# Performance work log

Measured on AMD Instinct MI355X. Metric: run time of the kernel, lower is better.

The kernel has to match this reference:

```python
import jax, jax.numpy as jnp
import numpy as np

B, N, D, C = 64, 512, 1024, 4  # batch, num_electrodes, d_model, num_classes
H = D // 2


def setup_inputs() -> dict:
    key = jax.random.key(0)
    ks = jax.random.split(key, 16)
    s = 0.02
    return {
        "Q": jax.random.normal(ks[0], (B, N, D), jnp.float32),
        "K": jax.random.normal(ks[1], (B, N, D), jnp.float32),
        "V": jax.random.normal(ks[2], (B, N, D), jnp.float32),
        "electrode_ids": jnp.arange(N, dtype=jnp.int64 if jax.config.jax_enable_x64 else jnp.int32),
        "emb": jax.random.normal(ks[3], (N, D), jnp.float32) * s,
        "dw1": jax.random.normal(ks[4], (H, D), jnp.float32) * s,
        "db1": jnp.zeros((H,), jnp.float32),
        "dw2": jax.random.normal(ks[5], (1, H), jnp.float32) * s,
        "db2": jnp.zeros((1,), jnp.float32),
        "sw1": jax.random.normal(ks[6], (H, D), jnp.float32) * s,
        "sb1": jnp.zeros((H,), jnp.float32),
        "sw2": jax.random.normal(ks[7], (1, H), jnp.float32) * s,
        "sb2": jnp.zeros((1,), jnp.float32),
        "dopamine_scale": jnp.asarray(1.0, jnp.float32),
        "serotonin_scale": jnp.asarray(1.0, jnp.float32),
        "fc_w": jax.random.normal(ks[8], (C, N * D), jnp.float32) * s,
        "fc_b": jnp.zeros((C,), jnp.float32),
    }


def reference(Q, K, V, electrode_ids, emb, dw1, db1, dw2, db2,
              sw1, sb1, sw2, sb2, dopamine_scale, serotonin_scale, fc_w, fc_b):
    e = emb[electrode_ids]                       # [N, D]
    Q = Q + e
    K = K + e
    V = V + e
    scale = jnp.sqrt(jnp.asarray(D, jnp.float32))
    scores = jnp.einsum('bnd,bmd->bnm', Q, K) / scale          # [B, N, N]
    probs = jax.nn.softmax(scores, axis=-1)
    entropy = -jnp.sum(probs * jnp.log(probs + 1e-6), axis=-1)  # [B, N]

    # dopamine MLP on Q tokens (eval mode -> dropout is identity)
    dh = jax.nn.relu(jnp.einsum('bnd,hd->bnh', Q, dw1) + db1)
    dopamine = jax.nn.sigmoid(jnp.einsum('bnh,oh->bno', dh, dw2) + db2)[..., 0]  # [B, N]

    # serotonin MLP on entropy broadcast to D identical features:
    # Linear(entropy * ones(D)) == entropy * W1.sum(axis=1) + b1 (same math, no [B,N,D] temp)
    sh = jax.nn.relu(entropy[..., None] * jnp.sum(sw1, axis=1) + sb1)            # [B, N, H]
    serotonin = jax.nn.sigmoid(jnp.einsum('bnh,oh->bno', sh, sw2) + sb2)[..., 0]  # [B, N]

    mod = dopamine_scale * dopamine[..., None] - serotonin_scale * serotonin[..., None]
    ms = scores + mod
    mu = jnp.mean(ms, axis=-1, keepdims=True)
    sd = jnp.std(ms, axis=-1, keepdims=True, ddof=1)  # torch.std default is unbiased
    ms = (ms - mu) / (sd + 1e-6)
    probs2 = jax.nn.softmax(ms, axis=-1)
    attn_out = jnp.einsum('bnm,bmd->bnd', probs2, V)   # [B, N, D]
    flat = attn_out.reshape(attn_out.shape[0], -1)      # [B, N*D]
    return flat @ fc_w.T + fc_b                          # [B, C]
```

## Files before the change

### kernel.cpp

```cpp
#include <hip/hip_runtime.h>

#define NN 512
#define ND 1024
#define NDW 524288
#define NBATCH 64

typedef __attribute__((ext_vector_type(8))) __bf16 bf16x8;
typedef __attribute__((ext_vector_type(4))) float f32x4;
typedef unsigned short u16;
typedef unsigned int u32;

__device__ __forceinline__ u16 f2bf(float x) {
    u32 u = __float_as_uint(x);
    u = (u + 0x7fffu + ((u >> 16) & 1u)) >> 16;
    return (u16)u;
}
__device__ __forceinline__ float bf2f(u16 x) {
    return __uint_as_float(((u32)x) << 16);
}

union BF8 { bf16x8 v; u16 s[8]; };

__device__ __forceinline__ void dma16(const u16* g, const u16* l) {
    __builtin_amdgcn_global_load_lds(
        (const __attribute__((address_space(1))) u32*)(uintptr_t)g,
        (__attribute__((address_space(3))) u32*)(u32)(uintptr_t)l,
        16, 0, 0);
}

__global__ __launch_bounds__(256)
void nma_init_out(float* __restrict__ out, const float* __restrict__ fcb) {
    int t = threadIdx.x;
    if (t < NBATCH * 4) out[t] = fcb[t & 3];
}

__global__ __launch_bounds__(256)
void prep_ke(const float* __restrict__ K, const int* __restrict__ eid,
             const float* __restrict__ emb, u16* __restrict__ Ke) {
    size_t f = ((size_t)blockIdx.x * 256 + threadIdx.x) * 8;
    int n = (int)((f >> 10) & (NN - 1));
    int col = (int)(f & (ND - 1));
    const float* kp = K + f;
    const float* ep = emb + (size_t)eid[n] * ND + col;
    float4 k0 = *(const float4*)kp, k1 = *(const float4*)(kp + 4);
    float4 e0 = *(const float4*)ep, e1 = *(const float4*)(ep + 4);
    union { uint4 q; u16 s[8]; } o;
    o.s[0]=f2bf(k0.x+e0.x); o.s[1]=f2bf(k0.y+e0.y); o.s[2]=f2bf(k0.z+e0.z); o.s[3]=f2bf(k0.w+e0.w);
    o.s[4]=f2bf(k1.x+e1.x); o.s[5]=f2bf(k1.y+e1.y); o.s[6]=f2bf(k1.z+e1.z); o.s[7]=f2bf(k1.w+e1.w);
    *(uint4*)(Ke + f) = o.q;
}

__global__ __launch_bounds__(256)
void prep_vt(const float* __restrict__ V, const int* __restrict__ eid,
             const float* __restrict__ emb, u16* __restrict__ VT) {
    __shared__ u16 T[64 * 72];
    const int tid = threadIdx.x;
    const int b = blockIdx.z, d0 = blockIdx.y * 64, n0 = blockIdx.x * 64;
    {
        const int r = tid >> 2, cs = (tid & 3) * 16;
        const int n = n0 + r;
        const float* vp = V + ((size_t)b * NN + n) * ND + d0 + cs;
        const float* ep = emb + (size_t)eid[n] * ND + d0 + cs;
        #pragma unroll
        for (int j = 0; j < 4; ++j) {
            float4 v = *(const float4*)(vp + j * 4);
            float4 e = *(const float4*)(ep + j * 4);
            T[(cs + j*4 + 0) * 72 + r] = f2bf(v.x + e.x);
            T[(cs + j*4 + 1) * 72 + r] = f2bf(v.y + e.y);
            T[(cs + j*4 + 2) * 72 + r] = f2bf(v.z + e.z);
            T[(cs + j*4 + 3) * 72 + r] = f2bf(v.w + e.w);
        }
    }
    __syncthreads();
    {
        const int dr = tid >> 2, ms = (tid & 3) * 16;
        u16* dst = VT + ((size_t)b * ND + d0 + dr) * NN + n0 + ms;
        *(uint4*)dst       = *(const uint4*)&T[dr * 72 + ms];
        *(uint4*)(dst + 8) = *(const uint4*)&T[dr * 72 + ms + 8];
    }
}

__global__ __launch_bounds__(256, 2)
void nma_attn(const float* __restrict__ Q, const int* __restrict__ eid,
              const float* __restrict__ emb, const u16* __restrict__ Ke,
              const u16* __restrict__ VT, u16* __restrict__ O)
{
    __shared__ __align__(16) u16 KV[NN * 32];
    __shared__ __align__(16) u16 Ps[32 * 520];
    __shared__ float red[4][32][4];
    __shared__ float rowM[32], rowInv[32], rowRden[32];

    const int tid  = threadIdx.x;
    const int w    = tid >> 6;
    const int lane = tid & 63;
    const int q    = lane >> 4;
    const int l15  = lane & 15;
    const int bid  = blockIdx.x;
    const int jj   = bid >> 3;
    const int b    = (bid & 7) + ((jj >> 4) << 3);
    const int i0   = (jj & 15) * 32;
    const size_t bOff = (size_t)b * NN * ND;

    const float* Qrow0 = Q + bOff + (size_t)(i0 + l15) * ND;
    const float* Qrow1 = Q + bOff + (size_t)(i0 + 16 + l15) * ND;
    const float* Erow0 = emb + (size_t)eid[i0 + l15] * ND;
    const float* Erow1 = emb + (size_t)eid[i0 + 16 + l15] * ND;

    const u16* KeB = Ke + bOff;
    const u16* VTB = VT + (size_t)b * ND * NN;
    const int liw = w * 64 + lane;

    f32x4 acc[2][8];
    #pragma unroll
    for (int it = 0; it < 2; ++it)
        #pragma unroll
        for (int mt = 0; mt < 8; ++mt)
            acc[it][mt] = (f32x4){0.f, 0.f, 0.f, 0.f};

    for (int kc = 0; kc < 32; ++kc) {
        __syncthreads();
        #pragma unroll
        for (int ii = 0; ii < 8; ++ii) {
            const int li = ii * 256 + liw;
            const int m = li >> 2, seg = li & 3;
            dma16(KeB + (size_t)m * ND + kc * 32 + seg * 8,
                  &KV[(size_t)(ii * 256 + w * 64) * 8]);
        }
        BF8 a0u, a1u;
        {
            const int k0 = kc * 32 + q * 8;
            float4 x0 = *(const float4*)(Qrow0 + k0);
            float4 x1 = *(const float4*)(Qrow0 + k0 + 4);
            float4 e0 = *(const float4*)(Erow0 + k0);
            float4 e1 = *(const float4*)(Erow0 + k0 + 4);
            a0u.s[0] = f2bf(x0.x + e0.x); a0u.s[1] = f2bf(x0.y + e0.y);
            a0u.s[2] = f2bf(x0.z + e0.z); a0u.s[3] = f2bf(x0.w + e0.w);
            a0u.s[4] = f2bf(x1.x + e1.x); a0u.s[5] = f2bf(x1.y + e1.y);
            a0u.s[6] = f2bf(x1.z + e1.z); a0u.s[7] = f2bf(x1.w + e1.w);
            x0 = *(const float4*)(Qrow1 + k0);
            x1 = *(const float4*)(Qrow1 + k0 + 4);
            e0 = *(const float4*)(Erow1 + k0);
            e1 = *(const float4*)(Erow1 + k0 + 4);
            a1u.s[0] = f2bf(x0.x + e0.x); a1u.s[1] = f2bf(x0.y + e0.y);
            a1u.s[2] = f2bf(x0.z + e0.z); a1u.s[3] = f2bf(x0.w + e0.w);
            a1u.s[4] = f2bf(x1.x + e1.x); a1u.s[5] = f2bf(x1.y + e1.y);
            a1u.s[6] = f2bf(x1.z + e1.z); a1u.s[7] = f2bf(x1.w + e1.w);
        }
        __syncthreads();
        #pragma unroll
        for (int mt = 0; mt < 8; ++mt) {
            bf16x8 bf = *(const bf16x8*)&KV[(w * 128 + mt * 16 + l15) * 32 + q * 8];
            acc[0][mt] = __builtin_amdgcn_mfma_f32_16x16x32_bf16(a0u.v, bf, acc[0][mt], 0, 0, 0);
            acc[1][mt] = __builtin_amdgcn_mfma_f32_16x16x32_bf16(a1u.v, bf, acc[1][mt], 0, 0, 0);
        }
    }

    const float SC = 0.03125f;
    #pragma unroll
    for (int it = 0; it < 2; ++it)
        #pragma unroll
        for (int mt = 0; mt < 8; ++mt) {
            acc[it][mt][0] *= SC; acc[it][mt][1] *= SC;
            acc[it][mt][2] *= SC; acc[it][mt][3] *= SC;
        }
    float ssum[2][4], ssq[2][4], smax[2][4];
    #pragma unroll
    for (int it = 0; it < 2; ++it)
        #pragma unroll
        for (int r = 0; r < 4; ++r) {
            float s = 0.f, s2 = 0.f, mx = -3.4e38f;
            #pragma unroll
            for (int mt = 0; mt < 8; ++mt) {
                float v = acc[it][mt][r];
                s += v; s2 += v * v; mx = fmaxf(mx, v);
            }
            #pragma unroll
            for (int d = 1; d < 16; d <<= 1) {
                s  += __shfl_xor(s, d);
                s2 += __shfl_xor(s2, d);
                mx  = fmaxf(mx, __shfl_xor(mx, d));
            }
            ssum[it][r] = s; ssq[it][r] = s2; smax[it][r] = mx;
        }
    if (l15 == 0) {
        #pragma unroll
        for (int it = 0; it < 2; ++it)
            #pragma unroll
            for (int r = 0; r < 4; ++r) {
                int i = it * 16 + q * 4 + r;
                red[w][i][0] = ssum[it][r];
                red[w][i][1] = ssq[it][r];
                red[w][i][2] = smax[it][r];
            }
    }
    __syncthreads();
    if (tid < 32) {
        float s  = red[0][tid][0] + red[1][tid][0] + red[2][tid][0] + red[3][tid][0];
        float s2 = red[0][tid][1] + red[1][tid][1] + red[2][tid][1] + red[3][tid][1];
        float mx = fmaxf(fmaxf(red[0][tid][2], red[1][tid][2]),
                         fmaxf(red[2][tid][2], red[3][tid][2]));
        float mu  = s * (1.f / 512.f);
        float var = fmaxf((s2 - s * mu) * (1.f / 511.f), 0.f);
        float sd  = sqrtf(var);
        rowM[tid]   = mx;
        rowInv[tid] = 1.f / (sd + 1e-6f);
    }
    __syncthreads();
    float dsum[2][4];
    #pragma unroll
    for (int it = 0; it < 2; ++it)
        #pragma unroll
        for (int r = 0; r < 4; ++r) {
            int i = it * 16 + q * 4 + r;
            float M = rowM[i], inv = rowInv[i];
            float s = 0.f;
            #pragma unroll
            for (int mt = 0; mt < 8; ++mt) {
                float e = __expf((acc[it][mt][r] - M) * inv);
                acc[it][mt][r] = e; s += e;
            }
            #pragma unroll
            for (int d = 1; d < 16; d <<= 1) s += __shfl_xor(s, d);
            dsum[it][r] = s;
        }
    if (l15 == 0) {
        #pragma unroll
        for (int it = 0; it < 2; ++it)
            #pragma unroll
            for (int r = 0; r < 4; ++r)
                red[w][it * 16 + q * 4 + r][0] = dsum[it][r];
    }
    __syncthreads();
    if (tid < 32)
        rowRden[tid] = 1.f / (red[0][tid][0] + red[1][tid][0] + red[2][tid][0] + red[3][tid][0]);
    __syncthreads();
    #pragma unroll
    for (int it = 0; it < 2; ++it)
        #pragma unroll
        for (int r = 0; r < 4; ++r) {
            int i = it * 16 + q * 4 + r;
            float rd = rowRden[i];
            #pragma unroll
            for (int mt = 0; mt < 8; ++mt) {
                int m = w * 128 + mt * 16 + l15;
                Ps[i * 520 + m] = f2bf(acc[it][mt][r] * rd);
            }
        }

    for (int h = 0; h < 2; ++h) {
        f32x4 oacc[2][8];
        #pragma unroll
        for (int it = 0; it < 2; ++it)
            #pragma unroll
            for (int dt = 0; dt < 8; ++dt)
                oacc[it][dt] = (f32x4){0.f, 0.f, 0.f, 0.f};
        for (int mc = 0; mc < 16; ++mc) {
            __syncthreads();
            #pragma unroll
            for (int ii = 0; ii < 8; ++ii) {
                const int li = ii * 256 + liw;
                const int r = li >> 2, seg = li & 3;
                dma16(VTB + (size_t)(h * 512 + r) * NN + mc * 32 + seg * 8,
                      &KV[(size_t)(ii * 256 + w * 64) * 8]);
            }
            __syncthreads();
            bf16x8 p0 = *(const bf16x8*)&Ps[l15 * 520 + mc * 32 + q * 8];
            bf16x8 p1 = *(const bf16x8*)&Ps[(16 + l15) * 520 + mc * 32 + q * 8];
            #pragma unroll
            for (int dt = 0; dt < 8; ++dt) {
                bf16x8 bf = *(const bf16x8*)&KV[(w * 128 + dt * 16 + l15) * 32 + q * 8];
                oacc[0][dt] = __builtin_amdgcn_mfma_f32_16x16x32_bf16(p0, bf, oacc[0][dt], 0, 0, 0);
                oacc[1][dt] = __builtin_amdgcn_mfma_f32_16x16x32_bf16(p1, bf, oacc[1][dt], 0, 0, 0);
            }
        }
        #pragma unroll
        for (int it = 0; it < 2; ++it)
            #pragma unroll
            for (int dt = 0; dt < 8; ++dt) {
                const int dglob = h * 512 + w * 128 + dt * 16 + l15;
                #pragma unroll
                for (int r = 0; r < 4; ++r) {
                    const int iglob = i0 + it * 16 + q * 4 + r;
                    O[bOff + (size_t)iglob * ND + dglob] = f2bf(oacc[it][dt][r]);
                }
            }
    }
}

__global__ __launch_bounds__(256)
void fc_red(const u16* __restrict__ O, const float* __restrict__ fcw,
            float* __restrict__ out)
{
    __shared__ __align__(16) u16 Osh[64 * 264];
    __shared__ __align__(16) float Fsh[4 * 260];
    const int tid = threadIdx.x;
    const size_t nbase = (size_t)blockIdx.x * 1024;
    const int b = tid >> 2, c = tid & 3;
    float sum = 0.f;
    for (int ch = 0; ch < 4; ++ch) {
        __syncthreads();
        #pragma unroll
        for (int ii = 0; ii < 8; ++ii) {
            int si = ii * 256 + tid;
            int row = si >> 5, col8 = (si & 31) * 8;
            *(uint4*)&Osh[row * 264 + col8] =
                *(const uint4*)(O + (size_t)row * NDW + nbase + ch * 256 + col8);
        }
        {
            int cc = tid >> 6, n4 = (tid & 63) * 4;
            *(float4*)&Fsh[cc * 260 + n4] =
                *(const float4*)(fcw + (size_t)cc * NDW + nbase + ch * 256 + n4);
        }
        __syncthreads();
        #pragma unroll 4
        for (int n8 = 0; n8 < 32; ++n8) {
            union { uint4 v; u16 s[8]; } o4;
            o4.v = *(const uint4*)&Osh[b * 264 + n8 * 8];
            float4 f0 = *(const float4*)&Fsh[c * 260 + n8 * 8];
            float4 f1 = *(const float4*)&Fsh[c * 260 + n8 * 8 + 4];
            sum += bf2f(o4.s[0]) * f0.x + bf2f(o4.s[1]) * f0.y
                 + bf2f(o4.s[2]) * f0.z + bf2f(o4.s[3]) * f0.w
                 + bf2f(o4.s[4]) * f1.x + bf2f(o4.s[5]) * f1.y
                 + bf2f(o4.s[6]) * f1.z + bf2f(o4.s[7]) * f1.w;
        }
    }
    atomicAdd(&out[b * 4 + c], sum);
}

extern "C" void kernel_launch(void* const* d_in, const int* in_sizes, int n_in,
                              void* d_out, int out_size, void* d_ws, size_t ws_size,
                              hipStream_t stream) {
    (void)in_sizes; (void)n_in; (void)ws_size; (void)out_size;
    const float* Q   = (const float*)d_in[0];
    const float* K   = (const float*)d_in[1];
    const float* V   = (const float*)d_in[2];
    const int*   eid = (const int*)d_in[3];
    const float* emb = (const float*)d_in[4];
    const float* fcw = (const float*)d_in[15];
    const float* fcb = (const float*)d_in[16];
    float* out = (float*)d_out;

    u16* Ke = (u16*)d_ws;
    u16* VT = Ke + (size_t)NBATCH * NN * ND;
    u16* O  = VT + (size_t)NBATCH * NN * ND;

    nma_init_out<<<dim3(1), dim3(256), 0, stream>>>(out, fcb);
    prep_ke<<<dim3(16384), dim3(256), 0, stream>>>(K, eid, emb, Ke);
    prep_vt<<<dim3(8, 16, 64), dim3(256), 0, stream>>>(V, eid, emb, VT);
    nma_attn<<<dim3(1024), dim3(256), 0, stream>>>(Q, eid, emb, Ke, VT, O);
    fc_red<<<dim3(512), dim3(256), 0, stream>>>(O, fcw, out);
}
```

Measured before the change: 742.9 us.

## Load K and V operands directly from global into registers, dropping LDS staging

```diff
diff --git a/kernel.cpp b/kernel.cpp
--- a/kernel.cpp
+++ b/kernel.cpp
@@ -20,13 +20,6 @@
 }
 
 union BF8 { bf16x8 v; u16 s[8]; };
-
-__device__ __forceinline__ void dma16(const u16* g, const u16* l) {
-    __builtin_amdgcn_global_load_lds(
-        (const __attribute__((address_space(1))) u32*)(uintptr_t)g,
-        (__attribute__((address_space(3))) u32*)(u32)(uintptr_t)l,
-        16, 0, 0);
-}
 
 __global__ __launch_bounds__(256)
 void nma_init_out(float* __restrict__ out, const float* __restrict__ fcb) {
@@ -80,12 +73,11 @@
     }
 }
 
-__global__ __launch_bounds__(256, 2)
+__global__ __launch_bounds__(256, 4)
 void nma_attn(const float* __restrict__ Q, const int* __restrict__ eid,
               const float* __restrict__ emb, const u16* __restrict__ Ke,
               const u16* __restrict__ VT, u16* __restrict__ O)
 {
-    __shared__ __align__(16) u16 KV[NN * 32];
     __shared__ __align__(16) u16 Ps[32 * 520];
     __shared__ float red[4][32][4];
     __shared__ float rowM[32], rowInv[32], rowRden[32];
@@ -106,9 +98,8 @@
     const float* Erow0 = emb + (size_t)eid[i0 + l15] * ND;
     const float* Erow1 = emb + (size_t)eid[i0 + 16 + l15] * ND;
 
-    const u16* KeB = Ke + bOff;
-    const u16* VTB = VT + (size_t)b * ND * NN;
-    const int liw = w * 64 + lane;
+    const u16* KeRow = Ke + bOff + (size_t)(w * 128 + l15) * ND + q * 8;
+    const u16* VTRow = VT + (size_t)b * ND * NN + (size_t)(w * 128 + l15) * NN + q * 8;
 
     f32x4 acc[2][8];
     #pragma unroll
@@ -118,17 +109,13 @@
             acc[it][mt] = (f32x4){0.f, 0.f, 0.f, 0.f};
 
     for (int kc = 0; kc < 32; ++kc) {
-        __syncthreads();
-        #pragma unroll
-        for (int ii = 0; ii < 8; ++ii) {
-            const int li = ii * 256 + liw;
-            const int m = li >> 2, seg = li & 3;
-            dma16(KeB + (size_t)m * ND + kc * 32 + seg * 8,
-                  &KV[(size_t)(ii * 256 + w * 64) * 8]);
-        }
+        const int k0 = kc * 32 + q * 8;
+        bf16x8 bv[8];
+        #pragma unroll
+        for (int mt = 0; mt < 8; ++mt)
+            bv[mt] = *(const bf16x8*)(KeRow + (size_t)mt * 16 * ND + kc * 32);
         BF8 a0u, a1u;
         {
-            const int k0 = kc * 32 + q * 8;
             float4 x0 = *(const float4*)(Qrow0 + k0);
             float4 x1 = *(const float4*)(Qrow0 + k0 + 4);
             float4 e0 = *(const float4*)(Erow0 + k0);
@@ -146,12 +133,10 @@
             a1u.s[4] = f2bf(x1.x + e1.x); a1u.s[5] = f2bf(x1.y + e1.y);
             a1u.s[6] = f2bf(x1.z + e1.z); a1u.s[7] = f2bf(x1.w + e1.w);
         }
-        __syncthreads();
         #pragma unroll
         for (int mt = 0; mt < 8; ++mt) {
-            bf16x8 bf = *(const bf16x8*)&KV[(w * 128 + mt * 16 + l15) * 32 + q * 8];
-            acc[0][mt] = __builtin_amdgcn_mfma_f32_16x16x32_bf16(a0u.v, bf, acc[0][mt], 0, 0, 0);
-            acc[1][mt] = __builtin_amdgcn_mfma_f32_16x16x32_bf16(a1u.v, bf, acc[1][mt], 0, 0, 0);
+            acc[0][mt] = __builtin_amdgcn_mfma_f32_16x16x32_bf16(a0u.v, bv[mt], acc[0][mt], 0, 0, 0);
+            acc[1][mt] = __builtin_amdgcn_mfma_f32_16x16x32_bf16(a1u.v, bv[mt], acc[1][mt], 0, 0, 0);
         }
     }
 
@@ -246,6 +231,7 @@
                 Ps[i * 520 + m] = f2bf(acc[it][mt][r] * rd);
             }
         }
+    __syncthreads();
 
     for (int h = 0; h < 2; ++h) {
         f32x4 oacc[2][8];
@@ -254,23 +240,18 @@
             #pragma unroll
             for (int dt = 0; dt < 8; ++dt)
                 oacc[it][dt] = (f32x4){0.f, 0.f, 0.f, 0.f};
+        const u16* VTh = VTRow + (size_t)h * 512 * NN;
         for (int mc = 0; mc < 16; ++mc) {
-            __syncthreads();
-            #pragma unroll
-            for (int ii = 0; ii < 8; ++ii) {
-                const int li = ii * 256 + liw;
-                const int r = li >> 2, seg = li & 3;
-                dma16(VTB + (size_t)(h * 512 + r) * NN + mc * 32 + seg * 8,
-                      &KV[(size_t)(ii * 256 + w * 64) * 8]);
-            }
-            __syncthreads();
+            bf16x8 bv[8];
+            #pragma unroll
+            for (int dt = 0; dt < 8; ++dt)
+                bv[dt] = *(const bf16x8*)(VTh + (size_t)dt * 16 * NN + mc * 32);
             bf16x8 p0 = *(const bf16x8*)&Ps[l15 * 520 + mc * 32 + q * 8];
             bf16x8 p1 = *(const bf16x8*)&Ps[(16 + l15) * 520 + mc * 32 + q * 8];
             #pragma unroll
             for (int dt = 0; dt < 8; ++dt) {
-                bf16x8 bf = *(const bf16x8*)&KV[(w * 128 + dt * 16 + l15) * 32 + q * 8];
-                oacc[0][dt] = __builtin_amdgcn_mfma_f32_16x16x32_bf16(p0, bf, oacc[0][dt], 0, 0, 0);
-                oacc[1][dt] = __builtin_amdgcn_mfma_f32_16x16x32_bf16(p1, bf, oacc[1][dt], 0, 0, 0);
+                oacc[0][dt] = __builtin_amdgcn_mfma_f32_16x16x32_bf16(p0, bv[dt], oacc[0][dt], 0, 0, 0);
+                oacc[1][dt] = __builtin_amdgcn_mfma_f32_16x16x32_bf16(p1, bv[dt], oacc[1][dt], 0, 0, 0);
             }
         }
         #pragma unroll
```

Result: slower. 877.8 us (+18.2%).
